# Optimization experiments

Hardware: AMD Instinct MI355X
Metric: run time of the kernel (lower is better)

The kernel has to match this reference:

```python
import jax, jax.numpy as jnp
import numpy as np

BLK = 8
COLOR_F = np.array([[0, 0.299, 0.587, 0.114],
                    [128, -0.168736, -0.331264, 0.5],
                    [128, 0.5, -0.418688, -0.081312]], dtype=np.float32)
COLOR_I = np.array([[-1.402 * 128, 1, 0, 1.402],
                    [1.058272 * 128, 1, -0.344136, -0.714136],
                    [-1.772 * 128, 1, 1.772, 0]], dtype=np.float32)
DCT_F = np.array([[0.3536, 0.3536, 0.3536, 0.3536, 0.3536, 0.3536, 0.3536, 0.3536],
                  [0.4904, 0.4157, 0.2778, 0.0975, -0.0975, -0.2778, -0.4157, -0.4904],
                  [0.4619, 0.1913, -0.1913, -0.4619, -0.4619, -0.1913, 0.1913, 0.4619],
                  [0.4157, -0.0975, -0.4904, -0.2778, 0.2778, 0.4904, 0.0975, -0.4157],
                  [0.3536, -0.3536, -0.3536, 0.3536, 0.3536, -0.3536, -0.3536, 0.3536],
                  [0.2778, -0.4904, 0.0975, 0.4157, -0.4157, -0.0975, 0.4904, -0.2778],
                  [0.1913, -0.4619, 0.4619, -0.1913, -0.1913, 0.4619, -0.4619, 0.1913],
                  [0.0975, -0.2778, 0.4157, -0.4904, 0.4904, -0.4157, 0.2778, -0.0975]], dtype=np.float32)

Q_LUMA_BASE = np.array([[16,11,10,16,24,40,51,61],[12,12,14,19,26,58,60,55],[14,13,16,24,40,57,69,56],[14,17,22,29,51,87,80,62],[18,22,37,56,68,109,103,77],[24,35,55,64,81,104,113,92],[49,64,78,87,103,121,120,101],[72,92,95,98,112,100,103,99]], dtype=np.float64)
Q_CHROMA_BASE = np.array([[17,18,24,47,99,99,99,99],[18,21,26,66,99,99,99,99],[24,26,56,99,99,99,99,99],[47,66,99,99,99,99,99,99],[99,99,99,99,99,99,99,99],[99,99,99,99,99,99,99,99],[99,99,99,99,99,99,99,99],[99,99,99,99,99,99,99,99]], dtype=np.float64)

def jpeg_qtable(quality, channel):
    # Standard IJG quality scaling
    base = Q_LUMA_BASE if channel == 0 else Q_CHROMA_BASE
    s = 5000.0 / quality if quality < 50 else 200.0 - 2.0 * quality
    q = np.floor((base * s + 50.0) / 100.0)
    return np.clip(q, 1, 255).astype(np.float32)

def _round_sin(x, steps=5):
    # Fourier-series approximation of round(x): x - sum_k (-1)^{k+1} sin(2*pi*k*x)/(pi*k)
    out = x
    for k in range(1, steps + 1):
        out = out - (((-1.0) ** (k + 1)) / (np.pi * k)) * jnp.sin((2.0 * np.pi * k) * x)
    return out

def setup_inputs() -> dict:
    key = jax.random.key(0)
    x = jax.random.uniform(key, (32, 512, 512, 3), dtype=jnp.float32)
    return {"x": x,
            "q_luma": jnp.asarray(jpeg_qtable(50, 0)),
            "q_chroma": jnp.asarray(jpeg_qtable(50, 1))}

def reference(x, q_luma, q_chroma):
    B, H, W, _ = x.shape
    F = jnp.asarray(DCT_F)
    cF0, cF = jnp.asarray(COLOR_F[:, 0]), jnp.asarray(COLOR_F[:, 1:])
    cI0, cI = jnp.asarray(COLOR_I[:, 0]), jnp.asarray(COLOR_I[:, 1:])
    # rgb -> ycbcr (affine color transform on 255*x with bias column)
    ycbcr = cF0 + 255.0 * jnp.einsum('bhwc,jc->bhwj', x, cF)
    # blocking: [B,3,H,W] -> [B,3,nblocks,8,8]
    p = jnp.transpose(ycbcr - 127.0, (0, 3, 1, 2))
    blocks = p.reshape(B, 3, H // BLK, BLK, W // BLK, BLK)
    blocks = jnp.transpose(blocks, (0, 1, 2, 4, 3, 5)).reshape(B, 3, -1, BLK, BLK)
    # 2D DCT per block: F @ b @ F^T
    X = jnp.einsum('ij,bcnjk,lk->bcnil', F, blocks, F)
    # per-channel quantization tables: channel 0 luma, channels 1,2 chroma
    Q = jnp.stack([q_luma, q_chroma, q_chroma])[:, None]  # [3,1,8,8]
    Xq = _round_sin(X / Q) * Q
    # IDCT per block: F^T @ Xq @ F
    ib = jnp.einsum('ji,bcnjk,kl->bcnil', F, Xq, F)
    # un-blocking back to [B,H,W,3]
    q = ib.reshape(B, 3, H // BLK, W // BLK, BLK, BLK)
    q = jnp.transpose(q, (0, 1, 2, 4, 3, 5)).reshape(B, 3, H, W)
    q = jnp.transpose(q, (0, 2, 3, 1))
    # ycbcr -> rgb
    y = (cI0 + jnp.einsum('bhwc,jc->bhwj', q + 127.0, cI)) / 255.0
    y = jnp.clip(y, 0.0, 1.0)
    return y, Xq.reshape(-1, BLK, BLK)
```

## Files before the change

### kernel.cpp

```cpp
#include <hip/hip_runtime.h>

#define IMG_H 512
#define IMG_W 512
#define NBATCH 32
#define BSTRIDE 68
#define PLANE (64*BSTRIDE)

static __device__ __forceinline__ float sin2pi(float x) {
    return __builtin_amdgcn_sinf(__builtin_amdgcn_fractf(x));
}

static __device__ __forceinline__ float clamp01(float v) {
    return fminf(fmaxf(v, 0.0f), 1.0f);
}

__global__ __launch_bounds__(192) void jpeg_fused_kernel(
    const float* __restrict__ x,
    const float* __restrict__ qL,
    const float* __restrict__ qC,
    float* __restrict__ out_y,
    float* __restrict__ out_xq)
{
    const float F8[8][8] = {
        {0.3536f,0.3536f,0.3536f,0.3536f,0.3536f,0.3536f,0.3536f,0.3536f},
        {0.4904f,0.4157f,0.2778f,0.0975f,-0.0975f,-0.2778f,-0.4157f,-0.4904f},
        {0.4619f,0.1913f,-0.1913f,-0.4619f,-0.4619f,-0.1913f,0.1913f,0.4619f},
        {0.4157f,-0.0975f,-0.4904f,-0.2778f,0.2778f,0.4904f,0.0975f,-0.4157f},
        {0.3536f,-0.3536f,-0.3536f,0.3536f,0.3536f,-0.3536f,-0.3536f,0.3536f},
        {0.2778f,-0.4904f,0.0975f,0.4157f,-0.4157f,-0.0975f,0.4904f,-0.2778f},
        {0.1913f,-0.4619f,0.4619f,-0.1913f,-0.1913f,0.4619f,-0.4619f,0.1913f},
        {0.0975f,-0.2778f,0.4157f,-0.4904f,0.4904f,-0.4157f,0.2778f,-0.0975f}};

    __shared__ __align__(16) float lds[3*PLANE];
    __shared__ float Qt[2][64];
    __shared__ float rQt[2][64];

    const int t = threadIdx.x;

    if (t < 64)       { float q = qL[t];    Qt[0][t]    = q; rQt[0][t]    = 1.0f/q; }
    else if (t < 128) { float q = qC[t-64]; Qt[1][t-64] = q; rQt[1][t-64] = 1.0f/q; }

    const int b   = blockIdx.y;
    const int th0 = (blockIdx.x >> 3) << 6;
    const int tw0 = (blockIdx.x & 7) << 6;

    const float* xb = x + (((size_t)b*IMG_H + th0) * IMG_W + tw0) * 3;

    #pragma unroll
    for (int it = 0; it < 6; ++it) {
        int q4 = it*192 + t;
        if (q4 < 1024) {
            int h = q4 >> 4, wq = q4 & 15;
            const float* p = xb + h*(IMG_W*3) + wq*12;
            float4 v0 = *(const float4*)(p);
            float4 v1 = *(const float4*)(p+4);
            float4 v2 = *(const float4*)(p+8);
            float px[4][3] = {{v0.x,v0.y,v0.z},{v0.w,v1.x,v1.y},
                              {v1.z,v1.w,v2.x},{v2.y,v2.z,v2.w}};
            float yc[3][4];
            #pragma unroll
            for (int i = 0; i < 4; ++i) {
                float r = px[i][0]*255.0f, g = px[i][1]*255.0f, bl = px[i][2]*255.0f;
                yc[0][i] = 0.299f*r + 0.587f*g + 0.114f*bl - 127.0f;
                yc[1][i] = 1.0f - 0.168736f*r - 0.331264f*g + 0.5f*bl;
                yc[2][i] = 1.0f + 0.5f*r - 0.418688f*g - 0.081312f*bl;
            }
            int bh = h >> 3, r8 = h & 7, bw = wq >> 1, qi = wq & 1;
            int base = (bh*8 + bw)*BSTRIDE + r8*8 + qi*4;
            #pragma unroll
            for (int c = 0; c < 3; ++c)
                *(float4*)&lds[c*PLANE + base] =
                    make_float4(yc[c][0], yc[c][1], yc[c][2], yc[c][3]);
        }
    }
    __syncthreads();

    {
        const int c   = t >> 6;
        const int blk = t & 63;
        float* Lb = &lds[(c*64 + blk)*BSTRIDE];

        float X[8][8];
        #pragma unroll
        for (int i = 0; i < 8; ++i) {
            float4 a  = *(const float4*)(Lb + i*8);
            float4 bb = *(const float4*)(Lb + i*8 + 4);
            X[i][0]=a.x;  X[i][1]=a.y;  X[i][2]=a.z;  X[i][3]=a.w;
            X[i][4]=bb.x; X[i][5]=bb.y; X[i][6]=bb.z; X[i][7]=bb.w;
        }
        #pragma unroll
        for (int i = 0; i < 8; ++i) {
            float row[8];
            #pragma unroll
            for (int k = 0; k < 8; ++k) row[k] = X[i][k];
            #pragma unroll
            for (int l = 0; l < 8; ++l) {
                float s = row[0]*F8[l][0];
                #pragma unroll
                for (int k = 1; k < 8; ++k) s += row[k]*F8[l][k];
                X[i][l] = s;
            }
        }
        #pragma unroll
        for (int l = 0; l < 8; ++l) {
            float col[8];
            #pragma unroll
            for (int j = 0; j < 8; ++j) col[j] = X[j][l];
            #pragma unroll
            for (int i = 0; i < 8; ++i) {
                float s = col[0]*F8[i][0];
                #pragma unroll
                for (int j = 1; j < 8; ++j) s += F8[i][j]*col[j];
                X[i][l] = s;
            }
        }
        const int qc = (c > 0) ? 1 : 0;
        #pragma unroll
        for (int i = 0; i < 8; ++i) {
            #pragma unroll
            for (int l = 0; l < 8; ++l) {
                float Q  = Qt[qc][i*8+l];
                float v  = X[i][l] * rQt[qc][i*8+l];
                float s  = v;
                s -=  0.3183098862f * sin2pi(v);
                s -= -0.1591549431f * sin2pi(2.0f*v);
                s -=  0.1061032954f * sin2pi(3.0f*v);
                s -= -0.0795774715f * sin2pi(4.0f*v);
                s -=  0.0636619772f * sin2pi(5.0f*v);
                X[i][l] = s * Q;
            }
        }
        {
            int bh = blk >> 3, bw = blk & 7;
            size_t xqbase = (((size_t)b*3 + c)*4096
                           + (size_t)((th0>>3) + bh)*64 + ((tw0>>3) + bw)) * 64;
            #pragma unroll
            for (int i = 0; i < 8; ++i) {
                *(float4*)(out_xq + xqbase + i*8)     = make_float4(X[i][0],X[i][1],X[i][2],X[i][3]);
                *(float4*)(out_xq + xqbase + i*8 + 4) = make_float4(X[i][4],X[i][5],X[i][6],X[i][7]);
            }
        }
        #pragma unroll
        for (int l = 0; l < 8; ++l) {
            float col[8];
            #pragma unroll
            for (int j = 0; j < 8; ++j) col[j] = X[j][l];
            #pragma unroll
            for (int i = 0; i < 8; ++i) {
                float s = F8[0][i]*col[0];
                #pragma unroll
                for (int j = 1; j < 8; ++j) s += F8[j][i]*col[j];
                X[i][l] = s;
            }
        }
        #pragma unroll
        for (int i = 0; i < 8; ++i) {
            float row[8];
            #pragma unroll
            for (int k = 0; k < 8; ++k) row[k] = X[i][k];
            #pragma unroll
            for (int l = 0; l < 8; ++l) {
                float s = row[0]*F8[0][l];
                #pragma unroll
                for (int k = 1; k < 8; ++k) s += row[k]*F8[k][l];
                X[i][l] = s;
            }
        }
        #pragma unroll
        for (int i = 0; i < 8; ++i) {
            *(float4*)(Lb + i*8)     = make_float4(X[i][0],X[i][1],X[i][2],X[i][3]);
            *(float4*)(Lb + i*8 + 4) = make_float4(X[i][4],X[i][5],X[i][6],X[i][7]);
        }
    }
    __syncthreads();

    float* yb = out_y + (((size_t)b*IMG_H + th0) * IMG_W + tw0) * 3;
    #pragma unroll
    for (int it = 0; it < 6; ++it) {
        int q4 = it*192 + t;
        if (q4 < 1024) {
            int h = q4 >> 4, wq = q4 & 15;
            int bh = h >> 3, r8 = h & 7, bw = wq >> 1, qi = wq & 1;
            int base = (bh*8 + bw)*BSTRIDE + r8*8 + qi*4;
            float4 vy = *(const float4*)&lds[0*PLANE + base];
            float4 vb = *(const float4*)&lds[1*PLANE + base];
            float4 vr = *(const float4*)&lds[2*PLANE + base];
            float Yv[4]={vy.x,vy.y,vy.z,vy.w};
            float Cb[4]={vb.x,vb.y,vb.z,vb.w};
            float Cr[4]={vr.x,vr.y,vr.z,vr.w};
            float o[4][3];
            #pragma unroll
            for (int i = 0; i < 4; ++i) {
                float yv = Yv[i] + 127.0f, cb = Cb[i] + 127.0f, cr = Cr[i] + 127.0f;
                o[i][0] = clamp01((-179.456f    + yv + 1.402f*cr) * (1.0f/255.0f));
                o[i][1] = clamp01(( 135.458816f + yv - 0.344136f*cb - 0.714136f*cr) * (1.0f/255.0f));
                o[i][2] = clamp01((-226.816f    + yv + 1.772f*cb) * (1.0f/255.0f));
            }
            float* p = yb + h*(IMG_W*3) + wq*12;
            *(float4*)(p)   = make_float4(o[0][0],o[0][1],o[0][2],o[1][0]);
            *(float4*)(p+4) = make_float4(o[1][1],o[1][2],o[2][0],o[2][1]);
            *(float4*)(p+8) = make_float4(o[2][2],o[3][0],o[3][1],o[3][2]);
        }
    }
}

extern "C" void kernel_launch(void* const* d_in, const int* in_sizes, int n_in,
                              void* d_out, int out_size, void* d_ws, size_t ws_size,
                              hipStream_t stream) {
    const float* x  = (const float*)d_in[0];
    const float* qL = (const float*)d_in[1];
    const float* qC = (const float*)d_in[2];
    float* out_y  = (float*)d_out;
    float* out_xq = (float*)d_out + (size_t)NBATCH*IMG_H*IMG_W*3;

    dim3 grid(64, NBATCH);
    dim3 block(192);
    jpeg_fused_kernel<<<grid, block, 0, stream>>>(x, qL, qC, out_y, out_xq);
}
```

Before: 312.2 us.

## Use even/odd butterfly DCT and Chebyshev sine recurrence for rounding

Replaces the dense 8x8 matrix-multiply DCT and IDCT with even/odd butterfly decompositions that exploit the symmetry of the DCT rows, cutting the multiply-adds per 1D transform. The five transcendental sin evaluations in the Fourier rounding approximation are replaced by one sin and one cos followed by the Chebyshev recurrence sin(kx) = 2cos(x)sin((k-1)x) - sin((k-2)x). Both aim to reduce ALU and transcendental-unit work per coefficient. The rounded DCT constants make the butterfly exact algebraically, but the recurrence and reassociation can shift float results slightly.

```diff
diff --git a/kernel.cpp b/kernel.cpp
--- a/kernel.cpp
+++ b/kernel.cpp
@@ -6,12 +6,42 @@
 #define BSTRIDE 68
 #define PLANE (64*BSTRIDE)
 
-static __device__ __forceinline__ float sin2pi(float x) {
-    return __builtin_amdgcn_sinf(__builtin_amdgcn_fractf(x));
-}
-
 static __device__ __forceinline__ float clamp01(float v) {
     return fminf(fmaxf(v, 0.0f), 1.0f);
+}
+
+static __device__ __forceinline__ void fwd8(const float in[8], float out[8]) {
+    const float p0 = in[0] + in[7], p1 = in[1] + in[6];
+    const float p2 = in[2] + in[5], p3 = in[3] + in[4];
+    const float m0 = in[0] - in[7], m1 = in[1] - in[6];
+    const float m2 = in[2] - in[5], m3 = in[3] - in[4];
+    const float a  = p0 + p3, bq = p1 + p2;
+    const float cd = p0 - p3, dd = p1 - p2;
+    out[0] = 0.3536f * (a + bq);
+    out[4] = 0.3536f * (a - bq);
+    out[2] = 0.4619f * cd + 0.1913f * dd;
+    out[6] = 0.1913f * cd - 0.4619f * dd;
+    out[1] = 0.4904f*m0 + 0.4157f*m1 + 0.2778f*m2 + 0.0975f*m3;
+    out[3] = 0.4157f*m0 - 0.0975f*m1 - 0.4904f*m2 - 0.2778f*m3;
+    out[5] = 0.2778f*m0 - 0.4904f*m1 + 0.0975f*m2 + 0.4157f*m3;
+    out[7] = 0.0975f*m0 - 0.2778f*m1 + 0.4157f*m2 - 0.4904f*m3;
+}
+
+static __device__ __forceinline__ void inv8(const float in[8], float out[8]) {
+    const float s04 = 0.3536f * (in[0] + in[4]);
+    const float d04 = 0.3536f * (in[0] - in[4]);
+    const float t0  = 0.4619f * in[2] + 0.1913f * in[6];
+    const float t1  = 0.1913f * in[2] - 0.4619f * in[6];
+    const float e0 = s04 + t0, e3 = s04 - t0;
+    const float e1 = d04 + t1, e2 = d04 - t1;
+    const float o0 = 0.4904f*in[1] + 0.4157f*in[3] + 0.2778f*in[5] + 0.0975f*in[7];
+    const float o1 = 0.4157f*in[1] - 0.0975f*in[3] - 0.4904f*in[5] - 0.2778f*in[7];
+    const float o2 = 0.2778f*in[1] - 0.4904f*in[3] + 0.0975f*in[5] + 0.4157f*in[7];
+    const float o3 = 0.0975f*in[1] - 0.2778f*in[3] + 0.4157f*in[5] - 0.4904f*in[7];
+    out[0] = e0 + o0;  out[7] = e0 - o0;
+    out[1] = e1 + o1;  out[6] = e1 - o1;
+    out[2] = e2 + o2;  out[5] = e2 - o2;
+    out[3] = e3 + o3;  out[4] = e3 - o3;
 }
 
 __global__ __launch_bounds__(192) void jpeg_fused_kernel(
@@ -21,16 +51,6 @@
     float* __restrict__ out_y,
     float* __restrict__ out_xq)
 {
-    const float F8[8][8] = {
-        {0.3536f,0.3536f,0.3536f,0.3536f,0.3536f,0.3536f,0.3536f,0.3536f},
-        {0.4904f,0.4157f,0.2778f,0.0975f,-0.0975f,-0.2778f,-0.4157f,-0.4904f},
-        {0.4619f,0.1913f,-0.1913f,-0.4619f,-0.4619f,-0.1913f,0.1913f,0.4619f},
-        {0.4157f,-0.0975f,-0.4904f,-0.2778f,0.2778f,0.4904f,0.0975f,-0.4157f},
-        {0.3536f,-0.3536f,-0.3536f,0.3536f,0.3536f,-0.3536f,-0.3536f,0.3536f},
-        {0.2778f,-0.4904f,0.0975f,0.4157f,-0.4157f,-0.0975f,0.4904f,-0.2778f},
-        {0.1913f,-0.4619f,0.4619f,-0.1913f,-0.1913f,0.4619f,-0.4619f,0.1913f},
-        {0.0975f,-0.2778f,0.4157f,-0.4904f,0.4904f,-0.4157f,0.2778f,-0.0975f}};
-
     __shared__ __align__(16) float lds[3*PLANE];
     __shared__ float Qt[2][64];
     __shared__ float rQt[2][64];
@@ -90,29 +110,21 @@
         }
         #pragma unroll
         for (int i = 0; i < 8; ++i) {
-            float row[8];
-            #pragma unroll
-            for (int k = 0; k < 8; ++k) row[k] = X[i][k];
-            #pragma unroll
-            for (int l = 0; l < 8; ++l) {
-                float s = row[0]*F8[l][0];
-                #pragma unroll
-                for (int k = 1; k < 8; ++k) s += row[k]*F8[l][k];
-                X[i][l] = s;
-            }
+            float tin[8], tout[8];
+            #pragma unroll
+            for (int k = 0; k < 8; ++k) tin[k] = X[i][k];
+            fwd8(tin, tout);
+            #pragma unroll
+            for (int l = 0; l < 8; ++l) X[i][l] = tout[l];
         }
         #pragma unroll
         for (int l = 0; l < 8; ++l) {
-            float col[8];
-            #pragma unroll
-            for (int j = 0; j < 8; ++j) col[j] = X[j][l];
-            #pragma unroll
-            for (int i = 0; i < 8; ++i) {
-                float s = col[0]*F8[i][0];
-                #pragma unroll
-                for (int j = 1; j < 8; ++j) s += F8[i][j]*col[j];
-                X[i][l] = s;
-            }
+            float tin[8], tout[8];
+            #pragma unroll
+            for (int j = 0; j < 8; ++j) tin[j] = X[j][l];
+            fwd8(tin, tout);
+            #pragma unroll
+            for (int i = 0; i < 8; ++i) X[i][l] = tout[i];
         }
         const int qc = (c > 0) ? 1 : 0;
         #pragma unroll
@@ -121,13 +133,18 @@
             for (int l = 0; l < 8; ++l) {
                 float Q  = Qt[qc][i*8+l];
                 float v  = X[i][l] * rQt[qc][i*8+l];
-                float s  = v;
-                s -=  0.3183098862f * sin2pi(v);
-                s -= -0.1591549431f * sin2pi(2.0f*v);
-                s -=  0.1061032954f * sin2pi(3.0f*v);
-                s -= -0.0795774715f * sin2pi(4.0f*v);
-                s -=  0.0636619772f * sin2pi(5.0f*v);
-                X[i][l] = s * Q;
+                float f  = __builtin_amdgcn_fractf(v);
+                float s1 = __builtin_amdgcn_sinf(f);
+                float c1 = __builtin_amdgcn_cosf(f);
+                float c2 = c1 + c1;
+                float s2 = c2*s1;
+                float s3 = c2*s2 - s1;
+                float s4 = c2*s3 - s2;
+                float s5 = c2*s4 - s3;
+                float r  = v - 0.3183098862f*s1 + 0.1591549431f*s2
+                             - 0.1061032954f*s3 + 0.0795774715f*s4
+                             - 0.0636619772f*s5;
+                X[i][l] = r * Q;
             }
         }
         {
@@ -142,29 +159,21 @@
         }
         #pragma unroll
         for (int l = 0; l < 8; ++l) {
-            float col[8];
-            #pragma unroll
-            for (int j = 0; j < 8; ++j) col[j] = X[j][l];
-            #pragma unroll
-            for (int i = 0; i < 8; ++i) {
-                float s = F8[0][i]*col[0];
-                #pragma unroll
-                for (int j = 1; j < 8; ++j) s += F8[j][i]*col[j];
-                X[i][l] = s;
-            }
-        }
-        #pragma unroll
-        for (int i = 0; i < 8; ++i) {
-            float row[8];
-            #pragma unroll
-            for (int k = 0; k < 8; ++k) row[k] = X[i][k];
-            #pragma unroll
-            for (int l = 0; l < 8; ++l) {
-                float s = row[0]*F8[0][l];
-                #pragma unroll
-                for (int k = 1; k < 8; ++k) s += row[k]*F8[k][l];
-                X[i][l] = s;
-            }
+            float tin[8], tout[8];
+            #pragma unroll
+            for (int j = 0; j < 8; ++j) tin[j] = X[j][l];
+            inv8(tin, tout);
+            #pragma unroll
+            for (int i = 0; i < 8; ++i) X[i][l] = tout[i];
+        }
+        #pragma unroll
+        for (int i = 0; i < 8; ++i) {
+            float tin[8], tout[8];
+            #pragma unroll
+            for (int k = 0; k < 8; ++k) tin[k] = X[i][k];
+            inv8(tin, tout);
+            #pragma unroll
+            for (int l = 0; l < 8; ++l) X[i][l] = tout[l];
         }
         #pragma unroll
         for (int i = 0; i < 8; ++i) {
```

Measured after the change: 310.7 us. No clear change (-0.5%).
